# Kernel tuning notes

Hardware: AMD Instinct MI355X
Metric: run time of the kernel (lower is better)

## Reference

```python
import jax, jax.numpy as jnp
import numpy as np

N = 50000
NFEAT = 512
HID = 128
E = 1_600_000


def spmm(row, col, val, dense):
    # sparse [N,N] (COO) @ dense [N,D] -> [N,D]
    gathered = val[:, None] * dense[col]           # [E, D]
    return jax.ops.segment_sum(gathered, row, num_segments=N)


def setup_inputs() -> dict:
    key = jax.random.key(0)
    ks = jax.random.split(key, 12)
    x = jax.random.normal(ks[0], (N, NFEAT), dtype=jnp.float32)
    adj_row = jax.random.randint(ks[1], (E,), 0, N, dtype=jnp.int32)
    adj_col = jax.random.randint(ks[2], (E,), 0, N, dtype=jnp.int32)
    adj_val = jax.random.uniform(ks[3], (E,), dtype=jnp.float32)
    adj_inv_row = jax.random.randint(ks[4], (E,), 0, N, dtype=jnp.int32)
    adj_inv_col = jax.random.randint(ks[5], (E,), 0, N, dtype=jnp.int32)
    adj_inv_val = jax.random.uniform(ks[6], (E,), dtype=jnp.float32)
    # Glorot-ish init for GCN weights
    W1 = jax.random.normal(ks[7], (NFEAT, HID), dtype=jnp.float32) * (1.0 / np.sqrt(NFEAT))
    b1 = jnp.zeros((HID,), dtype=jnp.float32)
    W2 = jax.random.normal(ks[8], (HID, NFEAT), dtype=jnp.float32) * (1.0 / np.sqrt(HID))
    b2 = jnp.zeros((NFEAT,), dtype=jnp.float32)
    return dict(x=x, adj_row=adj_row, adj_col=adj_col, adj_val=adj_val,
                adj_inv_row=adj_inv_row, adj_inv_col=adj_inv_col, adj_inv_val=adj_inv_val,
                W1=W1, b1=b1, W2=W2, b2=b2)


def reference(x, adj_row, adj_col, adj_val, adj_inv_row, adj_inv_col, adj_inv_val,
              W1, b1, W2, b2):
    # Encoder GCN layer: relu( adj @ (x @ W1) + b1 )
    h = jax.nn.relu(spmm(adj_row, adj_col, adj_val, x @ W1) + b1)   # [N, 128]
    embedding = h
    # Decoder GCN layer: relu( adj_inv @ (h @ W2) + b2 )
    out = jax.nn.relu(spmm(adj_inv_row, adj_inv_col, adj_inv_val, h @ W2) + b2)  # [N, nfeat]
    return (out, embedding)
```

## Files before the change

### kernel.cpp

```cpp
#include <hip/hip_runtime.h>

#define NN     50000
#define NFEAT  512
#define HIDD   128
#define NE     1600000
#define NB     ((NN + 255) / 256)

typedef __attribute__((ext_vector_type(8))) short    bf16x8;
typedef __attribute__((ext_vector_type(4))) float    f32x4;
typedef __attribute__((ext_vector_type(4))) unsigned short us4;

__device__ inline unsigned short f2bf(float f) {
  unsigned int u = __float_as_uint(f);
  u += 0x7FFFu + ((u >> 16) & 1u);
  return (unsigned short)(u >> 16);
}

__device__ inline float bf2f(unsigned short h) {
  return __uint_as_float((unsigned int)h << 16);
}

__device__ inline void fma4(float4& a, float v, const float4& d) {
  a.x = fmaf(v, d.x, a.x);
  a.y = fmaf(v, d.y, a.y);
  a.z = fmaf(v, d.z, a.z);
  a.w = fmaf(v, d.w, a.w);
}

__device__ inline void fma4b(float4& a, float v, us4 d) {
  a.x = fmaf(v, bf2f(d[0]), a.x);
  a.y = fmaf(v, bf2f(d[1]), a.y);
  a.z = fmaf(v, bf2f(d[2]), a.z);
  a.w = fmaf(v, bf2f(d[3]), a.w);
}

__global__ __launch_bounds__(256) void hist_rank_kernel(
    const int* __restrict__ rowA, const int* __restrict__ rowB,
    int* __restrict__ cntA, int* __restrict__ cntB,
    int* __restrict__ rnkA, int* __restrict__ rnkB, int e) {
  const int* row = blockIdx.y ? rowB : rowA;
  int*       cnt = blockIdx.y ? cntB : cntA;
  int*       rnk = blockIdx.y ? rnkB : rnkA;
  int i = blockIdx.x * 256 + threadIdx.x;
  if (i < e) rnk[i] = atomicAdd(&cnt[row[i]], 1);
}

__global__ __launch_bounds__(256) void block_sum_kernel(
    const int* __restrict__ cntA, const int* __restrict__ cntB,
    int* __restrict__ bsumA, int* __restrict__ bsumB, int n) {
  const int* counts = blockIdx.y ? cntB : cntA;
  int*       bsum   = blockIdx.y ? bsumB : bsumA;
  __shared__ int ws[4];
  int i = blockIdx.x * 256 + threadIdx.x;
  int lane = threadIdx.x & 63, wid = threadIdx.x >> 6;
  int v = (i < n) ? counts[i] : 0;
#pragma unroll
  for (int off = 32; off > 0; off >>= 1) v += __shfl_down(v, off, 64);
  if (lane == 0) ws[wid] = v;
  __syncthreads();
  if (threadIdx.x == 0) bsum[blockIdx.x] = ws[0] + ws[1] + ws[2] + ws[3];
}

__global__ __launch_bounds__(256) void scan_partials_kernel(
    int* __restrict__ bsumA, int* __restrict__ bsumB,
    int* __restrict__ rpA, int* __restrict__ rpB, int nb, int nfull) {
  int* bsum   = blockIdx.x ? bsumB : bsumA;
  int* rowptr = blockIdx.x ? rpB : rpA;
  __shared__ int ws[4];
  int t = threadIdx.x;
  int lane = t & 63, wid = t >> 6;
  int v = (t < nb) ? bsum[t] : 0;
  int incl = v;
#pragma unroll
  for (int off = 1; off < 64; off <<= 1) {
    int u = __shfl_up(incl, off, 64);
    if (lane >= off) incl += u;
  }
  if (lane == 63) ws[wid] = incl;
  __syncthreads();
  int wprefix = 0;
  for (int w = 0; w < wid; ++w) wprefix += ws[w];
  incl += wprefix;
  if (t < nb) bsum[t] = incl - v;
  if (t == nb - 1) rowptr[nfull] = incl;
}

__global__ __launch_bounds__(256) void scan_apply_kernel(
    const int* __restrict__ cntA, const int* __restrict__ cntB,
    const int* __restrict__ bsumA, const int* __restrict__ bsumB,
    int* __restrict__ rpA, int* __restrict__ rpB, int n) {
  const int* counts = blockIdx.y ? cntB : cntA;
  const int* bsum   = blockIdx.y ? bsumB : bsumA;
  int*       rowptr = blockIdx.y ? rpB : rpA;
  __shared__ int ws[4];
  int i = blockIdx.x * 256 + threadIdx.x;
  int lane = threadIdx.x & 63, wid = threadIdx.x >> 6;
  int v = (i < n) ? counts[i] : 0;
  int incl = v;
#pragma unroll
  for (int off = 1; off < 64; off <<= 1) {
    int u = __shfl_up(incl, off, 64);
    if (lane >= off) incl += u;
  }
  if (lane == 63) ws[wid] = incl;
  __syncthreads();
  int wprefix = 0;
  for (int w = 0; w < wid; ++w) wprefix += ws[w];
  if (i < n) rowptr[i] = bsum[blockIdx.x] + wprefix + (incl - v);
}

__global__ __launch_bounds__(256) void scatter_rank_kernel(
    const int* __restrict__ rowA, const int* __restrict__ colA,
    const float* __restrict__ valA, const int* __restrict__ rnkA,
    const int* __restrict__ rpA, int2* __restrict__ pairsA,
    const int* __restrict__ rowB, const int* __restrict__ colB,
    const float* __restrict__ valB, const int* __restrict__ rnkB,
    const int* __restrict__ rpB, int2* __restrict__ pairsB, int e) {
  const int*   row   = blockIdx.y ? rowB : rowA;
  const int*   col   = blockIdx.y ? colB : colA;
  const float* val   = blockIdx.y ? valB : valA;
  const int*   rnk   = blockIdx.y ? rnkB : rnkA;
  const int*   rp    = blockIdx.y ? rpB : rpA;
  int2*        pairs = blockIdx.y ? pairsB : pairsA;
  int i = blockIdx.x * 256 + threadIdx.x;
  if (i < e) {
    int p = rp[row[i]] + rnk[i];
    unsigned long long v =
        (unsigned long long)(unsigned int)col[i] |
        ((unsigned long long)(unsigned int)__float_as_uint(val[i]) << 32);
    atomicExch((unsigned long long*)&pairs[p], v);
  }
}

template <bool DB16, bool EPI, bool WF32, bool WB16>
__global__ __launch_bounds__(256) void spmm_kernel(
    const int* __restrict__ rowptr, const int2* __restrict__ pairs,
    const void* __restrict__ dense, const float* __restrict__ bias,
    float* __restrict__ outf, unsigned short* __restrict__ outb, int n) {
  int r = blockIdx.x * 8 + (threadIdx.x >> 5);
  if (r >= n) return;
  int c4 = (threadIdx.x & 31);
  int s = rowptr[r], e = rowptr[r + 1];
  float4 a0 = make_float4(0.f, 0.f, 0.f, 0.f);
  float4 a1 = a0, a2 = a0, a3 = a0;
  int j = s;
  if constexpr (DB16) {
    const unsigned short* d16 = (const unsigned short*)dense;
    for (; j + 8 <= e; j += 8) {
      int2 p0 = pairs[j + 0], p1 = pairs[j + 1], p2 = pairs[j + 2], p3 = pairs[j + 3];
      int2 p4 = pairs[j + 4], p5 = pairs[j + 5], p6 = pairs[j + 6], p7 = pairs[j + 7];
      us4 d0 = *(const us4*)(d16 + (size_t)p0.x * 128 + c4 * 4);
      us4 d1 = *(const us4*)(d16 + (size_t)p1.x * 128 + c4 * 4);
      us4 d2 = *(const us4*)(d16 + (size_t)p2.x * 128 + c4 * 4);
      us4 d3 = *(const us4*)(d16 + (size_t)p3.x * 128 + c4 * 4);
      us4 d4 = *(const us4*)(d16 + (size_t)p4.x * 128 + c4 * 4);
      us4 d5 = *(const us4*)(d16 + (size_t)p5.x * 128 + c4 * 4);
      us4 d6 = *(const us4*)(d16 + (size_t)p6.x * 128 + c4 * 4);
      us4 d7 = *(const us4*)(d16 + (size_t)p7.x * 128 + c4 * 4);
      fma4b(a0, __int_as_float(p0.y), d0);
      fma4b(a1, __int_as_float(p1.y), d1);
      fma4b(a2, __int_as_float(p2.y), d2);
      fma4b(a3, __int_as_float(p3.y), d3);
      fma4b(a0, __int_as_float(p4.y), d4);
      fma4b(a1, __int_as_float(p5.y), d5);
      fma4b(a2, __int_as_float(p6.y), d6);
      fma4b(a3, __int_as_float(p7.y), d7);
    }
    for (; j < e; ++j) {
      int2 ev = pairs[j];
      us4 d = *(const us4*)(d16 + (size_t)ev.x * 128 + c4 * 4);
      fma4b(a0, __int_as_float(ev.y), d);
    }
  } else {
    const float4* dense4 = (const float4*)dense;
    for (; j + 8 <= e; j += 8) {
      int2 p0 = pairs[j + 0], p1 = pairs[j + 1], p2 = pairs[j + 2], p3 = pairs[j + 3];
      int2 p4 = pairs[j + 4], p5 = pairs[j + 5], p6 = pairs[j + 6], p7 = pairs[j + 7];
      float4 d0 = dense4[(size_t)p0.x * 32 + c4];
      float4 d1 = dense4[(size_t)p1.x * 32 + c4];
      float4 d2 = dense4[(size_t)p2.x * 32 + c4];
      float4 d3 = dense4[(size_t)p3.x * 32 + c4];
      float4 d4 = dense4[(size_t)p4.x * 32 + c4];
      float4 d5 = dense4[(size_t)p5.x * 32 + c4];
      float4 d6 = dense4[(size_t)p6.x * 32 + c4];
      float4 d7 = dense4[(size_t)p7.x * 32 + c4];
      fma4(a0, __int_as_float(p0.y), d0);
      fma4(a1, __int_as_float(p1.y), d1);
      fma4(a2, __int_as_float(p2.y), d2);
      fma4(a3, __int_as_float(p3.y), d3);
      fma4(a0, __int_as_float(p4.y), d4);
      fma4(a1, __int_as_float(p5.y), d5);
      fma4(a2, __int_as_float(p6.y), d6);
      fma4(a3, __int_as_float(p7.y), d7);
    }
    for (; j < e; ++j) {
      int2 ev = pairs[j];
      float4 d = dense4[(size_t)ev.x * 32 + c4];
      fma4(a0, __int_as_float(ev.y), d);
    }
  }
  float4 acc;
  acc.x = (a0.x + a1.x) + (a2.x + a3.x);
  acc.y = (a0.y + a1.y) + (a2.y + a3.y);
  acc.z = (a0.z + a1.z) + (a2.z + a3.z);
  acc.w = (a0.w + a1.w) + (a2.w + a3.w);
  if (EPI) {
    float4 b = ((const float4*)bias)[c4];
    acc.x = fmaxf(acc.x + b.x, 0.f);
    acc.y = fmaxf(acc.y + b.y, 0.f);
    acc.z = fmaxf(acc.z + b.z, 0.f);
    acc.w = fmaxf(acc.w + b.w, 0.f);
  }
  if (WF32)
    *(float4*)(outf + (size_t)r * 128 + c4 * 4) = acc;
  if (WB16) {
    us4 h = {f2bf(acc.x), f2bf(acc.y), f2bf(acc.z), f2bf(acc.w)};
    *(us4*)(outb + (size_t)r * 128 + c4 * 4) = h;
  }
}

template <int K, int N, bool EPI, bool ABF16, bool OUTB>
__global__ __launch_bounds__(256) void gemm_mfma_kernel(
    const void* __restrict__ Av, const float* __restrict__ B,
    const float* __restrict__ bias, void* __restrict__ Cv, int M) {
  __shared__ __align__(16) unsigned short Alds[4096];
  __shared__ __align__(16) unsigned short Blds[4096];
  int tid = threadIdx.x;
  int lane = tid & 63, wid = tid >> 6;
  int wm = wid >> 1, wn = wid & 1;
  int rowBase = blockIdx.x * 128;
  int colBase = blockIdx.y * 128;
  int kg = tid & 7, mrow = tid >> 3;
  int aquad = kg >> 1, aj0 = (kg & 1) * 4;
  int bn = tid & 127, kh = tid >> 7;
  int NTb = bn >> 4, nloc = bn & 15;

  f32x4 acc[4][4];
#pragma unroll
  for (int mt = 0; mt < 4; ++mt)
#pragma unroll
    for (int nt = 0; nt < 4; ++nt)
      acc[mt][nt] = (f32x4){0.f, 0.f, 0.f, 0.f};

  for (int kb = 0; kb < K; kb += 32) {
    float4 av[4];
    us4 av16[4];
    if constexpr (ABF16) {
      const unsigned short* A = (const unsigned short*)Av;
#pragma unroll
      for (int p = 0; p < 4; ++p) {
        int r = rowBase + p * 32 + mrow;
        av16[p] = (r < M) ? *(const us4*)(A + (size_t)r * K + kb + kg * 4)
                          : (us4){0, 0, 0, 0};
      }
    } else {
      const float* A = (const float*)Av;
#pragma unroll
      for (int p = 0; p < 4; ++p) {
        int r = rowBase + p * 32 + mrow;
        av[p] = (r < M) ? *(const float4*)(A + (size_t)r * K + kb + kg * 4)
                        : make_float4(0.f, 0.f, 0.f, 0.f);
      }
    }
    float bv[4][4];
#pragma unroll
    for (int p = 0; p < 4; ++p) {
      int k = p * 8 + kh * 4;
#pragma unroll
      for (int i = 0; i < 4; ++i)
        bv[p][i] = B[(size_t)(kb + k + i) * N + colBase + bn];
    }
    __syncthreads();
#pragma unroll
    for (int p = 0; p < 4; ++p) {
      int m = p * 32 + mrow;
      int MT = m >> 4, mloc = m & 15;
      us4 h;
      if constexpr (ABF16) h = av16[p];
      else h = (us4){f2bf(av[p].x), f2bf(av[p].y), f2bf(av[p].z), f2bf(av[p].w)};
      *(us4*)&Alds[(((MT * 4 + aquad) * 16 + mloc) << 3) + aj0] = h;
    }
#pragma unroll
    for (int p = 0; p < 4; ++p) {
      us4 h = {f2bf(bv[p][0]), f2bf(bv[p][1]), f2bf(bv[p][2]), f2bf(bv[p][3])};
      *(us4*)&Blds[(((NTb * 4 + p) * 16 + nloc) << 3) + kh * 4] = h;
    }
    __syncthreads();
    bf16x8 af[4], bf[4];
#pragma unroll
    for (int mt = 0; mt < 4; ++mt)
      af[mt] = *(bf16x8*)&Alds[(((wm * 4 + mt) * 64 + lane)) << 3];
#pragma unroll
    for (int nt = 0; nt < 4; ++nt)
      bf[nt] = *(bf16x8*)&Blds[(((wn * 4 + nt) * 64 + lane)) << 3];
#pragma unroll
    for (int mt = 0; mt < 4; ++mt)
#pragma unroll
      for (int nt = 0; nt < 4; ++nt)
        acc[mt][nt] = __builtin_amdgcn_mfma_f32_16x16x32_bf16(
            af[mt], bf[nt], acc[mt][nt], 0, 0, 0);
  }
  int cquad = lane >> 4, cn = lane & 15;
#pragma unroll
  for (int nt = 0; nt < 4; ++nt) {
    int col = colBase + wn * 64 + nt * 16 + cn;
    float bb = EPI ? bias[col] : 0.f;
#pragma unroll
    for (int mt = 0; mt < 4; ++mt) {
      int r0 = rowBase + wm * 64 + mt * 16 + cquad * 4;
#pragma unroll
      for (int i = 0; i < 4; ++i) {
        int r = r0 + i;
        if (r < M) {
          float o = acc[mt][nt][i];
          if (EPI) o = fmaxf(o + bb, 0.f);
          if constexpr (OUTB)
            ((unsigned short*)Cv)[(size_t)r * N + col] = f2bf(o);
          else
            ((float*)Cv)[(size_t)r * N + col] = o;
        }
      }
    }
  }
}

extern "C" void kernel_launch(void* const* d_in, const int* in_sizes, int n_in,
                              void* d_out, int out_size, void* d_ws, size_t ws_size,
                              hipStream_t stream) {
  const float* x        = (const float*)d_in[0];
  const int*   adj_row  = (const int*)d_in[1];
  const int*   adj_col  = (const int*)d_in[2];
  const float* adj_val  = (const float*)d_in[3];
  const int*   ainv_row = (const int*)d_in[4];
  const int*   ainv_col = (const int*)d_in[5];
  const float* ainv_val = (const float*)d_in[6];
  const float* W1       = (const float*)d_in[7];
  const float* b1       = (const float*)d_in[8];
  const float* W2       = (const float*)d_in[9];
  const float* b2       = (const float*)d_in[10];

  float* out = (float*)d_out;
  float* emb = out + (size_t)NN * NFEAT;

  size_t off = 0;
  auto carve = [&](size_t bytes) {
    void* p = (char*)d_ws + off;
    off += (bytes + 255) & ~(size_t)255;
    return p;
  };
  unsigned short* Tb   = (unsigned short*)carve((size_t)NN * HIDD * 2);
  unsigned short* H0b  = (unsigned short*)carve((size_t)NN * HIDD * 2);
  int*  rowptr_a = (int*)carve(50004 * 4);
  int*  rowptr_b = (int*)carve(50004 * 4);
  int*  cnt_a    = (int*)carve(50004 * 4);
  int*  cnt_b    = (int*)carve(50004 * 4);
  int*  bsum_a   = (int*)carve(256 * 4);
  int*  bsum_b   = (int*)carve(256 * 4);
  int*  rank_a   = (int*)carve((size_t)NE * 4);
  int*  rank_b   = (int*)carve((size_t)NE * 4);
  int2* pairs_a  = (int2*)carve((size_t)NE * 8);
  int2* pairs_b  = (int2*)carve((size_t)NE * 8);
  unsigned short* embb = (unsigned short*)((char*)d_ws + off);
  bool full = ws_size >= off + (size_t)NN * HIDD * 2;

  hipMemsetAsync(cnt_a, 0, NN * sizeof(int), stream);
  hipMemsetAsync(cnt_b, 0, NN * sizeof(int), stream);
  hist_rank_kernel<<<dim3(NE / 256, 2), 256, 0, stream>>>(
      adj_row, ainv_row, cnt_a, cnt_b, rank_a, rank_b, NE);
  block_sum_kernel<<<dim3(NB, 2), 256, 0, stream>>>(cnt_a, cnt_b, bsum_a, bsum_b, NN);
  scan_partials_kernel<<<2, 256, 0, stream>>>(bsum_a, bsum_b, rowptr_a, rowptr_b,
                                              NB, NN);
  scan_apply_kernel<<<dim3(NB, 2), 256, 0, stream>>>(
      cnt_a, cnt_b, bsum_a, bsum_b, rowptr_a, rowptr_b, NN);
  scatter_rank_kernel<<<dim3(NE / 256, 2), 256, 0, stream>>>(
      adj_row, adj_col, adj_val, rank_a, rowptr_a, pairs_a,
      ainv_row, ainv_col, ainv_val, rank_b, rowptr_b, pairs_b, NE);

  gemm_mfma_kernel<NFEAT, HIDD, false, false, true>
      <<<dim3((NN + 127) / 128, 1), 256, 0, stream>>>(x, W1, nullptr, H0b, NN);

  if (full)
    spmm_kernel<true, true, true, true><<<(NN + 7) / 8, 256, 0, stream>>>(
        rowptr_a, pairs_a, H0b, b1, emb, embb, NN);
  else
    spmm_kernel<true, true, true, false><<<(NN + 7) / 8, 256, 0, stream>>>(
        rowptr_a, pairs_a, H0b, b1, emb, nullptr, NN);

  if (full)
    spmm_kernel<true, false, false, true><<<(NN + 7) / 8, 256, 0, stream>>>(
        rowptr_b, pairs_b, embb, nullptr, nullptr, Tb, NN);
  else
    spmm_kernel<false, false, false, true><<<(NN + 7) / 8, 256, 0, stream>>>(
        rowptr_b, pairs_b, emb, nullptr, nullptr, Tb, NN);

  gemm_mfma_kernel<HIDD, NFEAT, true, true, false>
      <<<dim3((NN + 127) / 128, 4), 256, 0, stream>>>(Tb, W2, b2, out, NN);
}
```

Before: 684.6 us.

## Split row histogram into eight sub-counters to cut atomic contention

The per-row edge counters are split into eight sub-histograms indexed by edge index modulo eight. The scan computes a per-sub-bucket base offset, and the scatter uses that base so each edge still gets a unique slot. The scatter also replaces its 64-bit atomic exchange with a plain store. This trades extra memset, read and write traffic on eight times larger count arrays for less same-address atomic contention. Edge order within a row changes, which can shift floating-point summation order.

Measured after the change: 634.6 us. 1.08x faster.

```diff
diff --git a/kernel.cpp b/kernel.cpp
--- a/kernel.cpp
+++ b/kernel.cpp
@@ -5,6 +5,7 @@
 #define HIDD   128
 #define NE     1600000
 #define NB     ((NN + 255) / 256)
+#define NSUB   8
 
 typedef __attribute__((ext_vector_type(8))) short    bf16x8;
 typedef __attribute__((ext_vector_type(4))) float    f32x4;
@@ -36,24 +37,31 @@
 
 __global__ __launch_bounds__(256) void hist_rank_kernel(
     const int* __restrict__ rowA, const int* __restrict__ rowB,
-    int* __restrict__ cntA, int* __restrict__ cntB,
+    int* __restrict__ cnt8A, int* __restrict__ cnt8B,
     int* __restrict__ rnkA, int* __restrict__ rnkB, int e) {
-  const int* row = blockIdx.y ? rowB : rowA;
-  int*       cnt = blockIdx.y ? cntB : cntA;
-  int*       rnk = blockIdx.y ? rnkB : rnkA;
+  const int* row  = blockIdx.y ? rowB : rowA;
+  int*       cnt8 = blockIdx.y ? cnt8B : cnt8A;
+  int*       rnk  = blockIdx.y ? rnkB : rnkA;
   int i = blockIdx.x * 256 + threadIdx.x;
-  if (i < e) rnk[i] = atomicAdd(&cnt[row[i]], 1);
+  if (i < e) {
+    int sub = i & (NSUB - 1);
+    rnk[i] = atomicAdd(&cnt8[sub * NN + row[i]], 1);
+  }
 }
 
 __global__ __launch_bounds__(256) void block_sum_kernel(
-    const int* __restrict__ cntA, const int* __restrict__ cntB,
+    const int* __restrict__ cnt8A, const int* __restrict__ cnt8B,
     int* __restrict__ bsumA, int* __restrict__ bsumB, int n) {
-  const int* counts = blockIdx.y ? cntB : cntA;
-  int*       bsum   = blockIdx.y ? bsumB : bsumA;
+  const int* cnt8 = blockIdx.y ? cnt8B : cnt8A;
+  int*       bsum = blockIdx.y ? bsumB : bsumA;
   __shared__ int ws[4];
   int i = blockIdx.x * 256 + threadIdx.x;
   int lane = threadIdx.x & 63, wid = threadIdx.x >> 6;
-  int v = (i < n) ? counts[i] : 0;
+  int v = 0;
+  if (i < n) {
+#pragma unroll
+    for (int s = 0; s < NSUB; ++s) v += cnt8[s * NN + i];
+  }
 #pragma unroll
   for (int off = 32; off > 0; off >>= 1) v += __shfl_down(v, off, 64);
   if (lane == 0) ws[wid] = v;
@@ -86,16 +94,23 @@
 }
 
 __global__ __launch_bounds__(256) void scan_apply_kernel(
-    const int* __restrict__ cntA, const int* __restrict__ cntB,
+    const int* __restrict__ cnt8A, const int* __restrict__ cnt8B,
     const int* __restrict__ bsumA, const int* __restrict__ bsumB,
-    int* __restrict__ rpA, int* __restrict__ rpB, int n) {
-  const int* counts = blockIdx.y ? cntB : cntA;
-  const int* bsum   = blockIdx.y ? bsumB : bsumA;
+    int* __restrict__ rpA, int* __restrict__ rpB,
+    int* __restrict__ sb8A, int* __restrict__ sb8B, int n) {
+  const int* cnt8 = blockIdx.y ? cnt8B : cnt8A;
+  const int* bsum = blockIdx.y ? bsumB : bsumA;
   int*       rowptr = blockIdx.y ? rpB : rpA;
+  int*       sb8  = blockIdx.y ? sb8B : sb8A;
   __shared__ int ws[4];
   int i = blockIdx.x * 256 + threadIdx.x;
   int lane = threadIdx.x & 63, wid = threadIdx.x >> 6;
-  int v = (i < n) ? counts[i] : 0;
+  int sc[NSUB];
+  int v = 0;
+  if (i < n) {
+#pragma unroll
+    for (int s = 0; s < NSUB; ++s) { sc[s] = cnt8[s * NN + i]; v += sc[s]; }
+  }
   int incl = v;
 #pragma unroll
   for (int off = 1; off < 64; off <<= 1) {
@@ -106,29 +121,32 @@
   __syncthreads();
   int wprefix = 0;
   for (int w = 0; w < wid; ++w) wprefix += ws[w];
-  if (i < n) rowptr[i] = bsum[blockIdx.x] + wprefix + (incl - v);
+  if (i < n) {
+    int base = bsum[blockIdx.x] + wprefix + (incl - v);
+    rowptr[i] = base;
+#pragma unroll
+    for (int s = 0; s < NSUB; ++s) { sb8[s * NN + i] = base; base += sc[s]; }
+  }
 }
 
 __global__ __launch_bounds__(256) void scatter_rank_kernel(
     const int* __restrict__ rowA, const int* __restrict__ colA,
     const float* __restrict__ valA, const int* __restrict__ rnkA,
-    const int* __restrict__ rpA, int2* __restrict__ pairsA,
+    const int* __restrict__ sb8A, int2* __restrict__ pairsA,
     const int* __restrict__ rowB, const int* __restrict__ colB,
     const float* __restrict__ valB, const int* __restrict__ rnkB,
-    const int* __restrict__ rpB, int2* __restrict__ pairsB, int e) {
+    const int* __restrict__ sb8B, int2* __restrict__ pairsB, int e) {
   const int*   row   = blockIdx.y ? rowB : rowA;
   const int*   col   = blockIdx.y ? colB : colA;
   const float* val   = blockIdx.y ? valB : valA;
   const int*   rnk   = blockIdx.y ? rnkB : rnkA;
-  const int*   rp    = blockIdx.y ? rpB : rpA;
+  const int*   sb8   = blockIdx.y ? sb8B : sb8A;
   int2*        pairs = blockIdx.y ? pairsB : pairsA;
   int i = blockIdx.x * 256 + threadIdx.x;
   if (i < e) {
-    int p = rp[row[i]] + rnk[i];
-    unsigned long long v =
-        (unsigned long long)(unsigned int)col[i] |
-        ((unsigned long long)(unsigned int)__float_as_uint(val[i]) << 32);
-    atomicExch((unsigned long long*)&pairs[p], v);
+    int sub = i & (NSUB - 1);
+    int p = sb8[sub * NN + row[i]] + rnk[i];
+    pairs[p] = make_int2(col[i], __float_as_int(val[i]));
   }
 }
 
@@ -352,8 +370,10 @@
   unsigned short* H0b  = (unsigned short*)carve((size_t)NN * HIDD * 2);
   int*  rowptr_a = (int*)carve(50004 * 4);
   int*  rowptr_b = (int*)carve(50004 * 4);
-  int*  cnt_a    = (int*)carve(50004 * 4);
-  int*  cnt_b    = (int*)carve(50004 * 4);
+  int*  cnt8_a   = (int*)carve((size_t)NSUB * NN * 4);
+  int*  cnt8_b   = (int*)carve((size_t)NSUB * NN * 4);
+  int*  sb8_a    = (int*)carve((size_t)NSUB * NN * 4);
+  int*  sb8_b    = (int*)carve((size_t)NSUB * NN * 4);
   int*  bsum_a   = (int*)carve(256 * 4);
   int*  bsum_b   = (int*)carve(256 * 4);
   int*  rank_a   = (int*)carve((size_t)NE * 4);
@@ -363,18 +383,18 @@
   unsigned short* embb = (unsigned short*)((char*)d_ws + off);
   bool full = ws_size >= off + (size_t)NN * HIDD * 2;
 
-  hipMemsetAsync(cnt_a, 0, NN * sizeof(int), stream);
-  hipMemsetAsync(cnt_b, 0, NN * sizeof(int), stream);
+  hipMemsetAsync(cnt8_a, 0, (size_t)NSUB * NN * sizeof(int), stream);
+  hipMemsetAsync(cnt8_b, 0, (size_t)NSUB * NN * sizeof(int), stream);
   hist_rank_kernel<<<dim3(NE / 256, 2), 256, 0, stream>>>(
-      adj_row, ainv_row, cnt_a, cnt_b, rank_a, rank_b, NE);
-  block_sum_kernel<<<dim3(NB, 2), 256, 0, stream>>>(cnt_a, cnt_b, bsum_a, bsum_b, NN);
+      adj_row, ainv_row, cnt8_a, cnt8_b, rank_a, rank_b, NE);
+  block_sum_kernel<<<dim3(NB, 2), 256, 0, stream>>>(cnt8_a, cnt8_b, bsum_a, bsum_b, NN);
   scan_partials_kernel<<<2, 256, 0, stream>>>(bsum_a, bsum_b, rowptr_a, rowptr_b,
                                               NB, NN);
   scan_apply_kernel<<<dim3(NB, 2), 256, 0, stream>>>(
-      cnt_a, cnt_b, bsum_a, bsum_b, rowptr_a, rowptr_b, NN);
+      cnt8_a, cnt8_b, bsum_a, bsum_b, rowptr_a, rowptr_b, sb8_a, sb8_b, NN);
   scatter_rank_kernel<<<dim3(NE / 256, 2), 256, 0, stream>>>(
-      adj_row, adj_col, adj_val, rank_a, rowptr_a, pairs_a,
-      ainv_row, ainv_col, ainv_val, rank_b, rowptr_b, pairs_b, NE);
+      adj_row, adj_col, adj_val, rank_a, sb8_a, pairs_a,
+      ainv_row, ainv_col, ainv_val, rank_b, sb8_b, pairs_b, NE);
 
   gemm_mfma_kernel<NFEAT, HIDD, false, false, true>
       <<<dim3((NN + 127) / 128, 1), 256, 0, stream>>>(x, W1, nullptr, H0b, NN);
```
